# Kernel optimization log

Hardware: AMD Instinct MI355X
Metric: run time of the kernel (lower is better)

## Reference

```python
import jax, jax.numpy as jnp
import numpy as np

# --- configuration (mirrors VFNet cfg) ---
B, NC = 1, 6                     # batch, surround cameras
C_IN, H_F, W_F = 64, 44, 80      # fused feature level (height//8, width//8)
XD, YD, ZD = 100, 100, 20        # voxel dims (x forward, inverse-depth spaced)
X0, X1 = 2.0, 51.5
Y0, Y1 = -25.0, 24.5
Z0, Z1 = -3.0, 2.7
DB, D_STR, D_END = 50, 2.0, 50.0 # projection depth bins (inverse-depth spaced)
VDIM, FOUT = 64, 256             # voxel_pre_dim, feat_out_dim
P = H_F * W_F
EPS = 1e-8


def _axes():
    ego_x = 1.0 / jnp.linspace(1.0 / X1, 1.0 / X0, XD)[::-1]  # ascending, nonuniform
    ego_y = jnp.linspace(Y0, Y1, YD)
    ego_z = jnp.linspace(Z0, Z1, ZD)
    return ego_x, ego_y, ego_z


def _voxel_pts():
    ex, ey, ez = _axes()
    gz, gy, gx = jnp.meshgrid(ez, ey, ex, indexing='ij')      # [Z,Y,X]
    pts = jnp.stack([gx, gy, gz], 0).reshape(3, -1)
    return jnp.concatenate([pts, jnp.ones((1, pts.shape[1]), pts.dtype)], 0)  # [4,N]


def _bilinear2d(img, u, v):
    C, H, W = img.shape
    u0, v0 = jnp.floor(u), jnp.floor(v)
    du, dv = u - u0, v - v0
    u0i = jnp.clip(u0.astype(jnp.int32), 0, W - 1); u1i = jnp.clip(u0i + 1, 0, W - 1)
    v0i = jnp.clip(v0.astype(jnp.int32), 0, H - 1); v1i = jnp.clip(v0i + 1, 0, H - 1)
    g = lambda vi, ui: img[:, vi, ui]
    return (g(v0i, u0i) * (1 - du) * (1 - dv) + g(v0i, u1i) * du * (1 - dv)
            + g(v1i, u0i) * (1 - du) * dv + g(v1i, u1i) * du * dv)


def _nonuniform_index(axis, q):
    # searchsorted + in-bin lerp: metric coord -> continuous index on nonuniform axis
    qc = jnp.clip(q, axis[0], axis[-1] - 1e-6)
    k = jnp.clip(jnp.searchsorted(axis, qc, side='left') - 1, 0, axis.shape[0] - 2)
    t = (qc - axis[k]) / (axis[k + 1] - axis[k] + 1e-12)
    return k.astype(qc.dtype) + t


def _trilinear(vol, xi, yi, zi):
    Cc, Zz, Yy, Xx = vol.shape
    def sp(i, n):
        i0 = jnp.floor(i); t = i - i0
        a = jnp.clip(i0.astype(jnp.int32), 0, n - 1)
        return a, jnp.clip(a + 1, 0, n - 1), t
    x0, x1, tx = sp(xi, Xx); y0, y1, ty = sp(yi, Yy); z0, z1, tz = sp(zi, Zz)
    g = lambda z, y, x: vol[:, z, y, x]
    c0 = (g(z0, y0, x0) * (1 - tx) + g(z0, y0, x1) * tx) * (1 - ty) + (g(z0, y1, x0) * (1 - tx) + g(z0, y1, x1) * tx) * ty
    c1 = (g(z1, y0, x0) * (1 - tx) + g(z1, y0, x1) * tx) * (1 - ty) + (g(z1, y1, x0) * (1 - tx) + g(z1, y1, x1) * tx) * ty
    return c0 * (1 - tz) + c1 * tz


def _conv2d(x, w, b):
    y = jax.lax.conv_general_dilated(x, w, (1, 1), 'SAME', dimension_numbers=('NCHW', 'OIHW', 'NCHW'))
    return y + b[None, :, None, None]


def _conv3d(x, w, b):
    y = jax.lax.conv_general_dilated(x, w, (1, 1, 1), 'SAME', dimension_numbers=('NCDHW', 'OIDHW', 'NCDHW'))
    return y + b[None, :, None, None, None]


def _forward(feats, masks, K, ext, w_ov, b_ov, w_no, b_no, w_fu, b_fu, w_r1, b_r1, w_r2, b_r2):
    ex, ey, ez = _axes()
    vpts = _voxel_pts()                                        # [4,N]
    fm = jnp.concatenate([feats[0], masks[0]], axis=1)         # [NC, C+1, H, W]
    ext_inv = jnp.linalg.inv(ext)

    # --- backproject surround-view features into the nonuniform voxel grid ---
    def per_cam(img, Kc, Ei):
        pix = Kc @ (Ei @ vpts)
        z = pix[2]
        u = pix[0] / (z + EPS); v = pix[1] / (z + EPS)
        valid = (z > EPS) & (u >= 0) & (u <= W_F - 1) & (v >= 0) & (v <= H_F - 1)
        return _bilinear2d(img, u, v) * valid, valid.astype(img.dtype)

    s, valid = jax.vmap(per_cam)(fm, K, ext_inv)               # [NC,C+1,N], [NC,N]
    count = valid.sum(0)
    cat = jnp.concatenate([s[:3].sum(0), s[3:].sum(0)], axis=0)  # [2*(C+1),N]
    ov = jax.nn.elu(w_ov @ cat + b_ov[:, None]) * (count == 2)
    no = jax.nn.elu(w_no @ s.sum(0) + b_no[:, None]) * (count == 1)
    vf = (ov + no).reshape(VDIM, ZD, YD, XD)                   # [64,Z,Y,X]

    # --- nonuniform-x -> uniform-x remap (searchsorted + lerp) + conv3d fusion ---
    xi_axis = _nonuniform_index(ex, jnp.linspace(X0, X1, XD))
    ZI, YI, XI = jnp.meshgrid(jnp.arange(ZD, dtype=vf.dtype), jnp.arange(YD, dtype=vf.dtype), xi_axis, indexing='ij')
    vf_remap = _trilinear(vf, XI, YI, ZI)
    vol = jax.nn.elu(_conv3d(jnp.concatenate([vf, vf_remap], 0)[None], w_fu, b_fu))[0]  # [64,Z,Y,X]

    # --- project fused voxel features into each camera frustum over inv-depth bins ---
    uu, vv = jnp.meshgrid(jnp.arange(W_F), jnp.arange(H_F), indexing='xy')
    pix_grid = jnp.stack([uu.reshape(-1).astype(feats.dtype), vv.reshape(-1).astype(feats.dtype), jnp.ones((P,), feats.dtype)], 0)  # [3,P]
    dbins = 1.0 / jnp.linspace(1.0 / D_END, 1.0 / D_STR, DB)[::-1]  # ascending, inv-depth spaced
    K3inv = jnp.linalg.inv(K[:, :3, :3])

    def per_cam_proj(Ki, Ec):
        dirs = Ki @ pix_grid                                   # [3,P]
        pc = dirs[:, None, :] * dbins[None, :, None]           # [3,D,P]
        pc = jnp.concatenate([pc, jnp.ones((1, DB, P), pc.dtype)], 0)
        pw = (Ec @ pc.reshape(4, -1)).reshape(4, DB, P)        # ego-frame points
        wx, wy, wz = pw[0], pw[1], pw[2]
        xi = _nonuniform_index(ex, wx)
        yi = (wy - Y0) / (Y1 - Y0) * (YD - 1)
        zi = (wz - Z0) / (Z1 - Z0) * (ZD - 1)
        inb = (wx >= X0) & (wx <= X1) & (yi >= 0) & (yi <= YD - 1) & (zi >= 0) & (zi <= ZD - 1)
        samp = _trilinear(vol, xi, yi, zi) * inb               # [64,D,P]
        return samp.reshape(VDIM * DB, H_F, W_F)

    proj = jax.vmap(per_cam_proj)(K3inv, ext)                  # [NC, 64*D, H, W]
    h = jax.nn.elu(_conv2d(proj, w_r1, b_r1))
    return jax.nn.elu(_conv2d(h, w_r2, b_r2))                  # [NC, 256, H, W]


def setup_inputs() -> dict:
    key = jax.random.key(0)
    ks = jax.random.split(key, 8)
    feats = jax.random.normal(ks[0], (B, NC, C_IN, H_F, W_F), jnp.float32)
    masks = jnp.ones((B, NC, 1, H_F, W_F), jnp.float32)
    Kn = np.eye(4, dtype=np.float32)
    Kn[0, 0] = Kn[1, 1] = 40.0; Kn[0, 2] = 40.0; Kn[1, 2] = 22.0  # ~90deg hfov at 80px
    K = np.tile(Kn, (NC, 1, 1))
    ext = np.zeros((NC, 4, 4), dtype=np.float32)
    for i in range(NC):
        th = 2 * np.pi * i / NC
        c, s0 = np.cos(th), np.sin(th)
        R = np.array([[s0, 0, c], [-c, 0, s0], [0, -1, 0]], dtype=np.float32)  # cam(right,down,fwd)->ego
        ext[i, :3, :3] = R
        ext[i, :3, 3] = np.array([c, s0, 0.8], dtype=np.float32)
        ext[i, 3, 3] = 1.0
    w_ov = jax.random.normal(ks[1], (VDIM, 2 * (C_IN + 1)), jnp.float32) / np.sqrt(2 * (C_IN + 1)).astype(np.float32)
    w_no = jax.random.normal(ks[2], (VDIM, C_IN + 1), jnp.float32) / np.sqrt(C_IN + 1).astype(np.float32)
    w_fu = jax.random.normal(ks[3], (VDIM, 2 * VDIM, 3, 3, 3), jnp.float32) / np.sqrt(2 * VDIM * 27).astype(np.float32)
    w_r1 = jax.random.normal(ks[4], (FOUT, VDIM * DB, 3, 3), jnp.float32) / np.sqrt(VDIM * DB * 9).astype(np.float32)
    w_r2 = jax.random.normal(ks[5], (FOUT, FOUT, 3, 3), jnp.float32) / np.sqrt(FOUT * 9).astype(np.float32)
    z = lambda n: jnp.zeros((n,), jnp.float32)
    return {"feats": feats, "masks": masks, "K": jnp.asarray(K), "ext": jnp.asarray(ext),
            "w_ov": w_ov, "b_ov": z(VDIM), "w_no": w_no, "b_no": z(VDIM),
            "w_fu": w_fu, "b_fu": z(VDIM), "w_r1": w_r1, "b_r1": z(FOUT),
            "w_r2": w_r2, "b_r2": z(FOUT)}


def reference(feats, masks, K, ext, w_ov, b_ov, w_no, b_no, w_fu, b_fu, w_r1, b_r1, w_r2, b_r2):
    return _forward(feats, masks, K, ext, w_ov, b_ov, w_no, b_no, w_fu, b_fu, w_r1, b_r1, w_r2, b_r2)
```

## Files before the change

### kernel.cpp

```cpp
#include <hip/hip_runtime.h>
#include <math.h>

#define NCAM 6
#define CIN  64
#define HF   44
#define WF   80
#define PP   (HF*WF)
#define XD   100
#define YD   100
#define ZD   20
#define NVOX (XD*YD*ZD)
#define DBN  50
#define VDIM 64
#define FOUT 256
#define EPSF 1e-8f

typedef _Float16 f16x4 __attribute__((ext_vector_type(4)));
typedef _Float16 f16x8 __attribute__((ext_vector_type(8)));
typedef float    f32x4 __attribute__((ext_vector_type(4)));

#define OFF_KE    0
#define OFF_K3I   96
#define OFF_XI    160
#define OFF_DBIN  260
#define OFF_WOVT  320
#define OFF_WNOT  8640
#define B_VOL     51200UL
#define B_WT1     51200UL
#define B_H       14796800UL
#define B_VIN     25651200UL
#define B_PROJ    25651200UL
#define B_WT2     25651200UL
#define B_WT3     76851200UL

__device__ __forceinline__ float eluf(float x) { return x > 0.f ? x : expm1f(x); }

#define AX_A    (1.0f/51.5f)
#define AX_STEP ((0.5f - 1.0f/51.5f)/99.0f)

__device__ __forceinline__ void inv3x3(const float m[9], float o[9]) {
    float a00 = m[4]*m[8] - m[5]*m[7];
    float a10 = m[5]*m[6] - m[3]*m[8];
    float a20 = m[3]*m[7] - m[4]*m[6];
    float det = m[0]*a00 + m[1]*a10 + m[2]*a20;
    float id = 1.0f/det;
    o[0] = a00*id;
    o[1] = (m[2]*m[7] - m[1]*m[8])*id;
    o[2] = (m[1]*m[5] - m[2]*m[4])*id;
    o[3] = a10*id;
    o[4] = (m[0]*m[8] - m[2]*m[6])*id;
    o[5] = (m[2]*m[3] - m[0]*m[5])*id;
    o[6] = a20*id;
    o[7] = (m[1]*m[6] - m[0]*m[7])*id;
    o[8] = (m[0]*m[4] - m[1]*m[3])*id;
}

__global__ __launch_bounds__(256) void setup_kernel(const float* K, const float* ext,
                                                    const float* w_ov, const float* w_no,
                                                    float* ws) {
    int t = threadIdx.x;
    if (t < NCAM) {
        const float* E = ext + t*16;
        float R[9] = {E[0],E[1],E[2], E[4],E[5],E[6], E[8],E[9],E[10]};
        float Ri[9];
        inv3x3(R, Ri);
        float tx=E[3], ty=E[7], tz=E[11];
        float bx = -(Ri[0]*tx + Ri[1]*ty + Ri[2]*tz);
        float by = -(Ri[3]*tx + Ri[4]*ty + Ri[5]*tz);
        float bz = -(Ri[6]*tx + Ri[7]*ty + Ri[8]*tz);
        float Ei[16] = {Ri[0],Ri[1],Ri[2],bx, Ri[3],Ri[4],Ri[5],by, Ri[6],Ri[7],Ri[8],bz, 0,0,0,1};
        const float* Km = K + t*16;
        float* KE = ws + OFF_KE + t*16;
        for (int r=0;r<4;r++)
            for (int c=0;c<4;c++) {
                float s=0.f;
                for (int k=0;k<4;k++) s += Km[r*4+k]*Ei[k*4+c];
                KE[r*4+c]=s;
            }
        float Kr[9] = {Km[0],Km[1],Km[2], Km[4],Km[5],Km[6], Km[8],Km[9],Km[10]};
        float Ki[9];
        inv3x3(Kr, Ki);
        float* KI = ws + OFF_K3I + t*9;
        for (int i=0;i<9;i++) KI[i]=Ki[i];
    }
    if (t >= 64 && t < 64+XD) {
        int x = t-64;
        float ex0 = 1.0f/(AX_A + 99.0f*AX_STEP);
        float exN = 1.0f/AX_A;
        float q = 2.0f + (float)x * (49.5f/99.0f);
        float qc = fminf(fmaxf(q, ex0), exN - 1e-6f);
        float f = 99.0f - (1.0f/qc - AX_A)/AX_STEP;
        int k = min(max((int)floorf(f),0),98);
        float exk  = 1.0f/(AX_A + (float)(99-k)*AX_STEP);
        float exk1 = 1.0f/(AX_A + (float)(98-k)*AX_STEP);
        ws[OFF_XI + x] = (float)k + (qc - exk)/(exk1 - exk + 1e-12f);
    }
    if (t >= 192 && t < 192+DBN) {
        int d = t-192;
        float sa = 1.0f/50.0f;
        float ss = (0.5f - sa)/49.0f;
        ws[OFF_DBIN + d] = 1.0f/(sa + (float)(49-d)*ss);
    }
    for (int i = t; i < 130*64; i += 256) {
        int k = i >> 6, c = i & 63;
        ws[OFF_WOVT + i] = w_ov[c*130 + k];
    }
    for (int i = t; i < 65*64; i += 256) {
        int k = i >> 6, c = i & 63;
        ws[OFF_WNOT + i] = w_no[c*65 + k];
    }
}

__global__ __launch_bounds__(256) void tw1_kernel(const float* w, _Float16* o) {
    int idx = blockIdx.x*256 + threadIdx.x;
    int cp  = idx % 3200;
    int oc  = (idx/3200) & 255;
    int tap = idx/(3200*256);
    int d = cp >> 6, v = cp & 63;
    o[idx] = (_Float16)w[((size_t)oc*3200 + v*50 + d)*9 + tap];
}
__global__ __launch_bounds__(256) void tw2_kernel(const float* w, _Float16* o) {
    int idx = blockIdx.x*256 + threadIdx.x;
    int ic  = idx & 255;
    int oc  = (idx >> 8) & 255;
    int tap = idx >> 16;
    o[idx] = (_Float16)w[((size_t)oc*256 + ic)*9 + tap];
}
__global__ __launch_bounds__(256) void tw3_kernel(const float* w, _Float16* o) {
    int idx = blockIdx.x*256 + threadIdx.x;
    int ci  = idx & 127;
    int oc  = (idx >> 7) & 63;
    int tap = idx >> 13;
    o[idx] = (_Float16)w[((size_t)oc*128 + ci)*27 + tap];
}

__global__ __launch_bounds__(256) void backproject_kernel(const float* feats, const float* masks,
                                                          const float* ws,
                                                          const float* b_ov, const float* b_no,
                                                          _Float16* vin) {
    int wave = threadIdx.x >> 6;
    int lane = threadIdx.x & 63;
    int n = blockIdx.x*4 + wave;
    int x = n % XD;
    int y = (n / XD) % YD;
    int z = n / (XD*YD);
    float gx = 1.0f/(AX_A + (float)(99-x)*AX_STEP);
    float gy = -25.0f + (float)y * (49.5f/99.0f);
    float gz = -3.0f  + (float)z * (5.7f/19.0f);

    float sA = 0.f, sB = 0.f, sA64 = 0.f, sB64 = 0.f;
    int cnt = 0;
    for (int cam = 0; cam < NCAM; ++cam) {
        const float* KE = ws + OFF_KE + cam*16;
        float px = KE[0]*gx + KE[1]*gy + KE[2]*gz + KE[3];
        float py = KE[4]*gx + KE[5]*gy + KE[6]*gz + KE[7];
        float pz = KE[8]*gx + KE[9]*gy + KE[10]*gz + KE[11];
        float inv = 1.0f/(pz + EPSF);
        float u = px*inv, v = py*inv;
        bool valid = (pz > EPSF) && (u >= 0.f) && (u <= 79.f) && (v >= 0.f) && (v <= 43.f);
        if (valid) {
            cnt++;
            float u0 = floorf(u), v0 = floorf(v);
            float du = u-u0, dv = v-v0;
            int u0i = min(max((int)u0,0),WF-1), u1i = min(u0i+1,WF-1);
            int v0i = min(max((int)v0,0),HF-1), v1i = min(v0i+1,HF-1);
            float w00=(1.f-du)*(1.f-dv), w01=du*(1.f-dv), w10=(1.f-du)*dv, w11=du*dv;
            int i00=v0i*WF+u0i, i01=v0i*WF+u1i, i10=v1i*WF+u0i, i11=v1i*WF+u1i;
            const float* img = feats + (cam*CIN + lane)*PP;
            float val = w00*img[i00] + w01*img[i01] + w10*img[i10] + w11*img[i11];
            const float* mg = masks + cam*PP;
            float mv = w00*mg[i00] + w01*mg[i01] + w10*mg[i10] + w11*mg[i11];
            if (cam < 3) { sA += val; sA64 += mv; }
            else         { sB += val; sB64 += mv; }
        }
    }
    float out = 0.f;
    if (cnt == 2) {
        const float* wT = ws + OFF_WOVT;
        float acc = b_ov[lane];
        for (int k = 0; k < 64; ++k) {
            float ca = __shfl(sA, k, 64);
            float cb = __shfl(sB, k, 64);
            acc += wT[k*64 + lane]*ca + wT[(65+k)*64 + lane]*cb;
        }
        acc += wT[64*64 + lane]*sA64 + wT[129*64 + lane]*sB64;
        out = eluf(acc);
    } else if (cnt == 1) {
        const float* wT = ws + OFF_WNOT;
        float s = sA + sB, s64 = sA64 + sB64;
        float acc = b_no[lane];
        for (int k = 0; k < 64; ++k) {
            float ca = __shfl(s, k, 64);
            acc += wT[k*64 + lane]*ca;
        }
        acc += wT[64*64 + lane]*s64;
        out = eluf(acc);
    }
    vin[(size_t)n*128 + lane] = (_Float16)out;
}

__global__ __launch_bounds__(256) void remap_kernel(const float* ws, _Float16* vin) {
    int wave = threadIdx.x >> 6, lane = threadIdx.x & 63;
    int n = blockIdx.x*4 + wave;
    int x = n % XD;
    float xi = ws[OFF_XI + x];
    float fx = floorf(xi);
    float t = xi - fx;
    int x0 = min(max((int)fx,0),XD-1);
    int x1 = min(x0+1, XD-1);
    size_t rowb = (size_t)(n - x)*128;
    float r = (float)vin[rowb + (size_t)x0*128 + lane]*(1.f-t)
            + (float)vin[rowb + (size_t)x1*128 + lane]*t;
    vin[(size_t)n*128 + 64 + lane] = (_Float16)r;
}

__global__ __launch_bounds__(256,2) void conv3d_mfma_kernel(const _Float16* __restrict__ vin,
                                                            const _Float16* __restrict__ wT,
                                                            const float* __restrict__ bias,
                                                            _Float16* __restrict__ vol) {
    __shared__ __align__(16) _Float16 Bs[9*104*36];
    int tid = threadIdx.x, lane = tid & 63, wave = tid >> 6;
    int ln = lane & 15, kq = lane >> 4;
    int y = blockIdx.x % 100, z = blockIdx.x / 100;
    int nt0 = wave*2;
    int ntn = (wave == 3) ? 1 : 2;
    f32x4 zero4 = {0.f,0.f,0.f,0.f};
    f32x4 acc[4][2];
    for (int i=0;i<4;i++) for (int t=0;t<2;t++) acc[i][t] = zero4;

    for (int c0 = 0; c0 < 128; c0 += 32) {
        __syncthreads();
        for (int g = tid; g < 9*104*4; g += 256) {
            int ic8 = g & 3;
            int xe  = (g >> 2) % 104;
            int rid = g / (104*4);
            int xx = xe - 1, yy = y + rid%3 - 1, zz = z + rid/3 - 1;
            f16x8 val = {0,0,0,0,0,0,0,0};
            if (xx >= 0 && xx < 100 && yy >= 0 && yy < 100 && zz >= 0 && zz < 20)
                val = *(const f16x8*)(vin + (size_t)((zz*100 + yy)*100 + xx)*128 + c0 + ic8*8);
            *(f16x8*)(&Bs[(rid*104 + xe)*36 + ic8*8]) = val;
        }
        __syncthreads();
        const _Float16* wp0 = wT + c0 + kq*8;
        f16x8 a0n = *(const f16x8*)(wp0 + (ln+ 0)*128);
        f16x8 a1n = *(const f16x8*)(wp0 + (ln+16)*128);
        f16x8 a2n = *(const f16x8*)(wp0 + (ln+32)*128);
        f16x8 a3n = *(const f16x8*)(wp0 + (ln+48)*128);
        for (int tap = 0; tap < 27; ++tap) {
            f16x8 a0 = a0n, a1 = a1n, a2 = a2n, a3 = a3n;
            if (tap < 26) {
                const _Float16* wp = wT + (size_t)(tap+1)*64*128 + c0 + kq*8;
                a0n = *(const f16x8*)(wp + (ln+ 0)*128);
                a1n = *(const f16x8*)(wp + (ln+16)*128);
                a2n = *(const f16x8*)(wp + (ln+32)*128);
                a3n = *(const f16x8*)(wp + (ln+48)*128);
            }
            int dx = tap % 3, rid = tap / 3;
            for (int t = 0; t < ntn; ++t) {
                int xe = min(16*(nt0+t) + ln + dx, 103);
                f16x8 b = *(const f16x8*)(&Bs[(rid*104 + xe)*36 + kq*8]);
                acc[0][t] = __builtin_amdgcn_mfma_f32_16x16x32_f16(a0, b, acc[0][t], 0,0,0);
                acc[1][t] = __builtin_amdgcn_mfma_f32_16x16x32_f16(a1, b, acc[1][t], 0,0,0);
                acc[2][t] = __builtin_amdgcn_mfma_f32_16x16x32_f16(a2, b, acc[2][t], 0,0,0);
                acc[3][t] = __builtin_amdgcn_mfma_f32_16x16x32_f16(a3, b, acc[3][t], 0,0,0);
            }
        }
    }
    for (int i = 0; i < 4; ++i) {
        int oc0 = i*16 + kq*4;
        f32x4 bv = *(const f32x4*)(bias + oc0);
        for (int t = 0; t < ntn; ++t) {
            int x = 16*(nt0+t) + ln;
            if (x < 100) {
                size_t n = (size_t)(z*100 + y)*100 + x;
                f16x4 s;
                s[0] = (_Float16)eluf(acc[i][t][0] + bv[0]);
                s[1] = (_Float16)eluf(acc[i][t][1] + bv[1]);
                s[2] = (_Float16)eluf(acc[i][t][2] + bv[2]);
                s[3] = (_Float16)eluf(acc[i][t][3] + bv[3]);
                *(f16x4*)(vol + n*64 + oc0) = s;
            }
        }
    }
}

__global__ __launch_bounds__(256) void project_kernel(const float* ws, const float* ext,
                                                      const _Float16* vol, _Float16* proj) {
    __shared__ unsigned s_off[256][8];
    __shared__ float    s_w[256][8];
    int tid = threadIdx.x;
    int item = blockIdx.x*256 + tid;
    int d = item % 50;
    int p = (item/50) % 3520;
    int cam = item / (50*3520);
    {
        float uu = (float)(p % WF), vv = (float)(p / WF);
        const float* KI = ws + OFF_K3I + cam*9;
        float dxr = KI[0]*uu + KI[1]*vv + KI[2];
        float dyr = KI[3]*uu + KI[4]*vv + KI[5];
        float dzr = KI[6]*uu + KI[7]*vv + KI[8];
        float dep = ws[OFF_DBIN + d];
        float cx = dxr*dep, cy = dyr*dep, cz = dzr*dep;
        const float* E = ext + cam*16;
        float wx = E[0]*cx + E[1]*cy + E[2]*cz  + E[3];
        float wy = E[4]*cx + E[5]*cy + E[6]*cz  + E[7];
        float wz = E[8]*cx + E[9]*cy + E[10]*cz + E[11];
        float ex0 = 1.0f/(AX_A + 99.0f*AX_STEP);
        float exN = 1.0f/AX_A;
        float qc = fminf(fmaxf(wx, ex0), exN - 1e-6f);
        float f = 99.0f - (1.0f/qc - AX_A)/AX_STEP;
        int k = min(max((int)floorf(f),0),98);
        float exk  = 1.0f/(AX_A + (float)(99-k)*AX_STEP);
        float exk1 = 1.0f/(AX_A + (float)(98-k)*AX_STEP);
        float xi = (float)k + (qc - exk)/(exk1 - exk + 1e-12f);
        float yi = (wy + 25.0f) * (99.0f/49.5f);
        float zi = (wz + 3.0f)  * (19.0f/5.7f);
        float scale = ((wx >= 2.0f) && (wx <= 51.5f) && (yi >= 0.f) && (yi <= 99.f)
                       && (zi >= 0.f) && (zi <= 19.f)) ? 1.f : 0.f;
        float fx = floorf(xi), fy = floorf(yi), fz = floorf(zi);
        float tx = xi-fx, ty = yi-fy, tz = zi-fz;
        int x0 = min(max((int)fx,0),XD-1), x1 = min(x0+1,XD-1);
        int y0 = min(max((int)fy,0),YD-1), y1 = min(y0+1,YD-1);
        int z0 = min(max((int)fz,0),ZD-1), z1 = min(z0+1,ZD-1);
        s_off[tid][0] = (unsigned)(((z0*YD+y0)*XD+x0)*64); s_w[tid][0] = (1.f-tx)*(1.f-ty)*(1.f-tz)*scale;
        s_off[tid][1] = (unsigned)(((z0*YD+y0)*XD+x1)*64); s_w[tid][1] = tx*(1.f-ty)*(1.f-tz)*scale;
        s_off[tid][2] = (unsigned)(((z0*YD+y1)*XD+x0)*64); s_w[tid][2] = (1.f-tx)*ty*(1.f-tz)*scale;
        s_off[tid][3] = (unsigned)(((z0*YD+y1)*XD+x1)*64); s_w[tid][3] = tx*ty*(1.f-tz)*scale;
        s_off[tid][4] = (unsigned)(((z1*YD+y0)*XD+x0)*64); s_w[tid][4] = (1.f-tx)*(1.f-ty)*tz*scale;
        s_off[tid][5] = (unsigned)(((z1*YD+y0)*XD+x1)*64); s_w[tid][5] = tx*(1.f-ty)*tz*scale;
        s_off[tid][6] = (unsigned)(((z1*YD+y1)*XD+x0)*64); s_w[tid][6] = (1.f-tx)*ty*tz*scale;
        s_off[tid][7] = (unsigned)(((z1*YD+y1)*XD+x1)*64); s_w[tid][7] = tx*ty*tz*scale;
    }
    __syncthreads();
    int wave = tid >> 6, lane = tid & 63;
    size_t outbase = (size_t)blockIdx.x*256 + wave*64;
    for (int j = 0; j < 64; ++j) {
        int it = wave*64 + j;
        float a = 0.f;
        #pragma unroll
        for (int c = 0; c < 8; ++c)
            a += s_w[it][c] * (float)vol[s_off[it][c] + lane];
        proj[(outbase + j)*64 + lane] = (_Float16)a;
    }
}

template<int ICN, bool OUT16>
__global__ __launch_bounds__(256,2) void conv2d_mfma_kernel(const _Float16* __restrict__ in,
                                                            const _Float16* __restrict__ wT,
                                                            const float* __restrict__ bias,
                                                            void* __restrict__ outp) {
    constexpr int NCH = ICN/32;
    constexpr int NSLOT = 6;
    __shared__ __align__(16) _Float16 Bs[2][4*82*36];
    int tid = threadIdx.x, lane = tid & 63, wave = tid >> 6;
    int wm = wave >> 1, wn = wave & 1;
    int ln = lane & 15, kq = lane >> 4;
    int bid = blockIdx.x;
    int ocq = bid & 3;
    int rest = bid >> 2;
    int cam = rest % 6;
    int h0 = (rest / 6)*2;
    int ocb = ocq*64 + wm*32;
    size_t campix0 = (size_t)cam*3520;
    f32x4 zero4 = {0.f,0.f,0.f,0.f};
    f32x4 acc[2][5];
    for (int i=0;i<2;i++) for (int t=0;t<5;t++) acc[i][t] = zero4;

    size_t soff[NSLOT];
    int    slds[NSLOT];
    bool   sok[NSLOT];
    #pragma unroll
    for (int i = 0; i < NSLOT; ++i) {
        int g = tid + i*256;
        if (g < 4*82*4) {
            int ic8 = g & 3;
            int we  = (g >> 2) % 82;
            int re  = g / (82*4);
            int h = h0 - 1 + re;
            int w = we - 1;
            sok[i]  = (h >= 0 && h < HF && w >= 0 && w < WF);
            soff[i] = (campix0 + h*80 + w)*(size_t)ICN + ic8*8;
            slds[i] = (re*82 + we)*36 + ic8*8;
        } else { sok[i] = false; soff[i] = 0; slds[i] = -1; }
    }

    f16x8 sreg[NSLOT];
    #pragma unroll
    for (int i = 0; i < NSLOT; ++i) {
        f16x8 v = {0,0,0,0,0,0,0,0};
        if (sok[i]) v = *(const f16x8*)(in + soff[i]);
        sreg[i] = v;
    }

    const _Float16* wbase0 = wT + (size_t)ocb*ICN + kq*8;
    for (int c = 0; c < NCH; ++c) {
        int buf = c & 1;
        #pragma unroll
        for (int i = 0; i < NSLOT; ++i)
            if (slds[i] >= 0) *(f16x8*)(&Bs[buf][slds[i]]) = sreg[i];
        __syncthreads();
        if (c + 1 < NCH) {
            int c1 = (c+1)*32;
            #pragma unroll
            for (int i = 0; i < NSLOT; ++i) {
                f16x8 v = {0,0,0,0,0,0,0,0};
                if (sok[i]) v = *(const f16x8*)(in + soff[i] + c1);
                sreg[i] = v;
            }
        }
        f16x8 A0[9], A1[9];
        const _Float16* wb = wbase0 + c*32;
        #pragma unroll
        for (int tap = 0; tap < 9; ++tap) {
            const _Float16* wp = wb + (size_t)tap*256*ICN;
            A0[tap] = *(const f16x8*)(wp + (size_t)(ln+ 0)*ICN);
            A1[tap] = *(const f16x8*)(wp + (size_t)(ln+16)*ICN);
        }
        #pragma unroll
        for (int tap = 0; tap < 9; ++tap) {
            int ky = tap/3, kx = tap%3;
            int rbase = (wn + ky)*82 + ln + kx;
            #pragma unroll
            for (int t = 0; t < 5; ++t) {
                f16x8 b = *(const f16x8*)(&Bs[buf][(rbase + 16*t)*36 + kq*8]);
                acc[0][t] = __builtin_amdgcn_mfma_f32_16x16x32_f16(A0[tap], b, acc[0][t], 0,0,0);
                acc[1][t] = __builtin_amdgcn_mfma_f32_16x16x32_f16(A1[tap], b, acc[1][t], 0,0,0);
            }
        }
    }
    int pixrow = h0 + wn;
    for (int i = 0; i < 2; ++i) {
        int oc0 = ocb + i*16 + kq*4;
        f32x4 bv = *(const f32x4*)(bias + oc0);
        for (int t = 0; t < 5; ++t) {
            int pix = pixrow*80 + 16*t + ln;
            float v0 = eluf(acc[i][t][0] + bv[0]);
            float v1 = eluf(acc[i][t][1] + bv[1]);
            float v2 = eluf(acc[i][t][2] + bv[2]);
            float v3 = eluf(acc[i][t][3] + bv[3]);
            if (OUT16) {
                f16x4 s; s[0]=(_Float16)v0; s[1]=(_Float16)v1; s[2]=(_Float16)v2; s[3]=(_Float16)v3;
                *(f16x4*)((_Float16*)outp + (campix0 + pix)*256 + oc0) = s;
            } else {
                float* op = (float*)outp + ((size_t)(cam*256 + oc0))*PP + pix;
                op[0] = v0; op[PP] = v1; op[2*PP] = v2; op[3*PP] = v3;
            }
        }
    }
}

extern "C" void kernel_launch(void* const* d_in, const int* in_sizes, int n_in,
                              void* d_out, int out_size, void* d_ws, size_t ws_size,
                              hipStream_t stream) {
    const float* feats = (const float*)d_in[0];
    const float* masks = (const float*)d_in[1];
    const float* K     = (const float*)d_in[2];
    const float* ext   = (const float*)d_in[3];
    const float* w_ov  = (const float*)d_in[4];
    const float* b_ov  = (const float*)d_in[5];
    const float* w_no  = (const float*)d_in[6];
    const float* b_no  = (const float*)d_in[7];
    const float* w_fu  = (const float*)d_in[8];
    const float* b_fu  = (const float*)d_in[9];
    const float* w_r1  = (const float*)d_in[10];
    const float* b_r1  = (const float*)d_in[11];
    const float* w_r2  = (const float*)d_in[12];
    const float* b_r2  = (const float*)d_in[13];
    char* base = (char*)d_ws;
    float*    wsf  = (float*)base;
    _Float16* vol  = (_Float16*)(base + B_VOL);
    _Float16* wT1  = (_Float16*)(base + B_WT1);
    _Float16* h    = (_Float16*)(base + B_H);
    _Float16* vin  = (_Float16*)(base + B_VIN);
    _Float16* proj = (_Float16*)(base + B_PROJ);
    _Float16* wT2  = (_Float16*)(base + B_WT2);
    _Float16* wT3  = (_Float16*)(base + B_WT3);
    float* out = (float*)d_out;

    setup_kernel<<<1, 256, 0, stream>>>(K, ext, w_ov, w_no, wsf);
    tw3_kernel<<<(27*64*128)/256, 256, 0, stream>>>(w_fu, wT3);
    backproject_kernel<<<NVOX/4, 256, 0, stream>>>(feats, masks, wsf, b_ov, b_no, vin);
    remap_kernel<<<NVOX/4, 256, 0, stream>>>(wsf, vin);
    conv3d_mfma_kernel<<<ZD*YD, 256, 0, stream>>>(vin, wT3, b_fu, vol);
    project_kernel<<<(NCAM*PP*DBN)/256, 256, 0, stream>>>(wsf, ext, vol, proj);
    tw1_kernel<<<(9*256*3200)/256, 256, 0, stream>>>(w_r1, wT1);
    conv2d_mfma_kernel<3200, true><<<4*NCAM*22, 256, 0, stream>>>(proj, wT1, b_r1, h);
    tw2_kernel<<<(9*256*256)/256, 256, 0, stream>>>(w_r2, wT2);
    conv2d_mfma_kernel<256, false><<<4*NCAM*22, 256, 0, stream>>>(h, wT2, b_r2, out);
}
```

Baseline: 1.753 ms.

## Split backprojection into gather pass and MFMA-based per-voxel MLP kernel

Backprojection now only gathers per-camera-group feature sums into an fp16 staging buffer of 160 columns per voxel. A separate kernel then runs both linear layers (overlap and non-overlap weights stacked into 128 rows) as one MFMA GEMM, picking the right output by camera count. This replaces the per-lane shuffle-based scalar matvec, at the cost of an extra pass through a 200k x 160 fp16 buffer and reduced-precision inputs and weights.

```diff
diff --git a/kernel.cpp b/kernel.cpp
--- a/kernel.cpp
+++ b/kernel.cpp
@@ -32,6 +32,9 @@
 #define B_PROJ    25651200UL
 #define B_WT2     25651200UL
 #define B_WT3     76851200UL
+#define B_S       77294592UL
+#define B_W2      141294592UL
+#define SK        160
 
 __device__ __forceinline__ float eluf(float x) { return x > 0.f ? x : expm1f(x); }
 
@@ -101,14 +104,6 @@
         float ss = (0.5f - sa)/49.0f;
         ws[OFF_DBIN + d] = 1.0f/(sa + (float)(49-d)*ss);
     }
-    for (int i = t; i < 130*64; i += 256) {
-        int k = i >> 6, c = i & 63;
-        ws[OFF_WOVT + i] = w_ov[c*130 + k];
-    }
-    for (int i = t; i < 65*64; i += 256) {
-        int k = i >> 6, c = i & 63;
-        ws[OFF_WNOT + i] = w_no[c*65 + k];
-    }
 }
 
 __global__ __launch_bounds__(256) void tw1_kernel(const float* w, _Float16* o) {
@@ -133,11 +128,29 @@
     int tap = idx >> 13;
     o[idx] = (_Float16)w[((size_t)oc*128 + ci)*27 + tap];
 }
-
-__global__ __launch_bounds__(256) void backproject_kernel(const float* feats, const float* masks,
-                                                          const float* ws,
-                                                          const float* b_ov, const float* b_no,
-                                                          _Float16* vin) {
+__global__ __launch_bounds__(256) void tw4_kernel(const float* w_ov, const float* w_no,
+                                                  _Float16* o) {
+    int idx = blockIdx.x*256 + threadIdx.x;
+    int k = idx % SK;
+    int r = idx / SK;
+    float v = 0.f;
+    if (r < 64) {
+        if (k < 64)                 v = w_ov[r*130 + k];
+        else if (k == 64)           v = w_ov[r*130 + 64];
+        else if (k >= 66 && k < 130) v = w_ov[r*130 + 65 + (k-66)];
+        else if (k == 130)          v = w_ov[r*130 + 129];
+    } else {
+        int rr = r - 64;
+        if (k < 64)                 v = w_no[rr*65 + k];
+        else if (k == 64)           v = w_no[rr*65 + 64];
+        else if (k >= 66 && k < 130) v = w_no[rr*65 + (k-66)];
+        else if (k == 130)          v = w_no[rr*65 + 64];
+    }
+    o[idx] = (_Float16)v;
+}
+
+__global__ __launch_bounds__(256) void gather_kernel(const float* feats, const float* masks,
+                                                     const float* ws, _Float16* S) {
     int wave = threadIdx.x >> 6;
     int lane = threadIdx.x & 63;
     int n = blockIdx.x*4 + wave;
@@ -174,29 +187,72 @@
             else         { sB += val; sB64 += mv; }
         }
     }
-    float out = 0.f;
-    if (cnt == 2) {
-        const float* wT = ws + OFF_WOVT;
-        float acc = b_ov[lane];
-        for (int k = 0; k < 64; ++k) {
-            float ca = __shfl(sA, k, 64);
-            float cb = __shfl(sB, k, 64);
-            acc += wT[k*64 + lane]*ca + wT[(65+k)*64 + lane]*cb;
-        }
-        acc += wT[64*64 + lane]*sA64 + wT[129*64 + lane]*sB64;
-        out = eluf(acc);
-    } else if (cnt == 1) {
-        const float* wT = ws + OFF_WNOT;
-        float s = sA + sB, s64 = sA64 + sB64;
-        float acc = b_no[lane];
-        for (int k = 0; k < 64; ++k) {
-            float ca = __shfl(s, k, 64);
-            acc += wT[k*64 + lane]*ca;
-        }
-        acc += wT[64*64 + lane]*s64;
-        out = eluf(acc);
-    }
-    vin[(size_t)n*128 + lane] = (_Float16)out;
+    _Float16* Sp = S + (size_t)n*SK;
+    Sp[lane]      = (_Float16)sA;
+    Sp[66 + lane] = (_Float16)sB;
+    if (lane == 0) { Sp[64] = (_Float16)sA64; Sp[130] = (_Float16)sB64; }
+    if (lane == 1) Sp[65] = (_Float16)0.f;
+    if (lane >= 3 && lane <= 30) Sp[131 + (lane-3)] = (_Float16)0.f;
+    if (lane == 31) Sp[159] = (_Float16)(float)cnt;
+}
+
+__global__ __launch_bounds__(256,2) void mlp_kernel(const _Float16* __restrict__ S,
+                                                    const _Float16* __restrict__ W2,
+                                                    const float* __restrict__ b_ov,
+                                                    const float* __restrict__ b_no,
+                                                    _Float16* __restrict__ vin) {
+    constexpr int WPAD = 168;
+    __shared__ __align__(16) _Float16 Wl[128*WPAD];
+    int tid = threadIdx.x, lane = tid & 63, wave = tid >> 6;
+    int ln = lane & 15, kq = lane >> 4;
+    for (int i = tid; i < 128*20; i += 256) {
+        int r = i / 20, g8 = i % 20;
+        *(f16x8*)(&Wl[r*WPAD + g8*8]) = *(const f16x8*)(W2 + r*SK + g8*8);
+    }
+    __syncthreads();
+
+    int nbase = blockIdx.x*128 + wave*32;
+    f32x4 zero4 = {0.f,0.f,0.f,0.f};
+    f32x4 acc[8][2];
+    for (int m=0;m<8;m++) for (int t=0;t<2;t++) acc[m][t] = zero4;
+
+    for (int ks = 0; ks < 5; ++ks) {
+        int k0 = ks*32 + kq*8;
+        f16x8 b0, b1;
+        {
+            int c0 = min(nbase + ln,      NVOX-1);
+            int c1 = min(nbase + 16 + ln, NVOX-1);
+            b0 = *(const f16x8*)(S + (size_t)c0*SK + k0);
+            b1 = *(const f16x8*)(S + (size_t)c1*SK + k0);
+        }
+        #pragma unroll
+        for (int m = 0; m < 8; ++m) {
+            f16x8 a = *(const f16x8*)(&Wl[(m*16 + ln)*WPAD + k0]);
+            acc[m][0] = __builtin_amdgcn_mfma_f32_16x16x32_f16(a, b0, acc[m][0], 0,0,0);
+            acc[m][1] = __builtin_amdgcn_mfma_f32_16x16x32_f16(a, b1, acc[m][1], 0,0,0);
+        }
+    }
+    #pragma unroll
+    for (int t = 0; t < 2; ++t) {
+        int col = nbase + t*16 + ln;
+        if (col >= NVOX) continue;
+        float cnt = (float)S[(size_t)col*SK + 159];
+        #pragma unroll
+        for (int m = 0; m < 4; ++m) {
+            int oc0 = m*16 + kq*4;
+            f32x4 bov = *(const f32x4*)(b_ov + oc0);
+            f32x4 bno = *(const f32x4*)(b_no + oc0);
+            f16x4 s;
+            #pragma unroll
+            for (int r = 0; r < 4; ++r) {
+                float v = 0.f;
+                if (cnt == 2.f)      v = eluf(acc[m][t][r]   + bov[r]);
+                else if (cnt == 1.f) v = eluf(acc[m+4][t][r] + bno[r]);
+                s[r] = (_Float16)v;
+            }
+            *(f16x4*)(vin + (size_t)col*128 + oc0) = s;
+        }
+    }
 }
 
 __global__ __launch_bounds__(256) void remap_kernel(const float* ws, _Float16* vin) {
@@ -475,11 +531,15 @@
     _Float16* proj = (_Float16*)(base + B_PROJ);
     _Float16* wT2  = (_Float16*)(base + B_WT2);
     _Float16* wT3  = (_Float16*)(base + B_WT3);
+    _Float16* Sbuf = (_Float16*)(base + B_S);
+    _Float16* W2   = (_Float16*)(base + B_W2);
     float* out = (float*)d_out;
 
     setup_kernel<<<1, 256, 0, stream>>>(K, ext, w_ov, w_no, wsf);
     tw3_kernel<<<(27*64*128)/256, 256, 0, stream>>>(w_fu, wT3);
-    backproject_kernel<<<NVOX/4, 256, 0, stream>>>(feats, masks, wsf, b_ov, b_no, vin);
+    tw4_kernel<<<(128*SK)/256, 256, 0, stream>>>(w_ov, w_no, W2);
+    gather_kernel<<<NVOX/4, 256, 0, stream>>>(feats, masks, wsf, Sbuf);
+    mlp_kernel<<<(NVOX + 127)/128, 256, 0, stream>>>(Sbuf, W2, b_ov, b_no, vin);
     remap_kernel<<<NVOX/4, 256, 0, stream>>>(wsf, vin);
     conv3d_mfma_kernel<<<ZD*YD, 256, 0, stream>>>(vin, wT3, b_fu, vol);
     project_kernel<<<(NCAM*PP*DBN)/256, 256, 0, stream>>>(wsf, ext, vol, proj);
```

New measurement: 1.674 ms. 4.5% less time.
